# Kernel tuning notes

Measured on AMD Instinct MI355X. Metric: run time of the kernel, lower is better.

Reference implementation:

```python
import jax, jax.numpy as jnp
import numpy as np

B, S, D, H = 4, 1024, 1024, 16
HD = D // H  # head_dim = 64


def setup_inputs() -> dict:
    key = jax.random.key(0)
    ks = jax.random.split(key, 12)
    inp = {
        "query": jax.random.normal(ks[0], (B, S, D), jnp.float32),
        "key": jax.random.normal(ks[1], (B, S, D), jnp.float32),
        "value": jax.random.normal(ks[2], (B, S, D), jnp.float32),
        # padding mask: 0 = masked, 1 = keep; broadcastable to [B,H,Sq,Sk]
        "mask": jax.random.randint(ks[3], (B, 1, 1, S), 0, 2, jnp.int32),
        # Dense params (Glorot-ish scale)
        "Wq": jax.random.normal(ks[4], (D, D), jnp.float32) / np.sqrt(D),
        "bq": jnp.zeros((D,), jnp.float32),
        "Wk": jax.random.normal(ks[5], (D, D), jnp.float32) / np.sqrt(D),
        "bk": jnp.zeros((D,), jnp.float32),
        "Wv": jax.random.normal(ks[6], (D, D), jnp.float32) / np.sqrt(D),
        "bv": jnp.zeros((D,), jnp.float32),
        "Wo": jax.random.normal(ks[7], (D, D), jnp.float32) / np.sqrt(D),
        "bo": jnp.zeros((D,), jnp.float32),
    }
    return inp


def _split_heads(x):
    # [B, S, D] -> [B, H, S, HD]
    b, s, _ = x.shape
    return x.reshape(b, s, H, HD).transpose(0, 2, 1, 3)


def reference(query, key, value, mask, Wq, bq, Wk, bk, Wv, bv, Wo, bo):
    q = _split_heads(query @ Wq + bq)   # [B,H,S,HD]
    k = _split_heads(key @ Wk + bk)
    v = _split_heads(value @ Wv + bv)

    scale = jnp.sqrt(jnp.asarray(HD, q.dtype))
    energy = jnp.einsum("bhqd,bhkd->bhqk", q, k) / scale  # [B,H,S,S]
    energy = jnp.where(mask == 0, jnp.asarray(-1e10, energy.dtype), energy)
    attention = jax.nn.softmax(energy, axis=-1)
    # dropout is identity at inference
    x = jnp.einsum("bhqk,bhkd->bhqd", attention, v)       # [B,H,S,HD]
    x = x.transpose(0, 2, 1, 3).reshape(query.shape[0], -1, H * HD)  # [B,S,D]
    outputs = x @ Wo + bo
    return outputs, attention
```

## Files before the change

### kernel.cpp

```cpp
#include <hip/hip_runtime.h>

typedef short short8  __attribute__((ext_vector_type(8)));
typedef short short4v __attribute__((ext_vector_type(4)));
typedef float float4v __attribute__((ext_vector_type(4)));
typedef int   int4v   __attribute__((ext_vector_type(4)));

__device__ __forceinline__ short f2bf(float f) {
    unsigned u = __builtin_bit_cast(unsigned, f);
    u += 0x7fff + ((u >> 16) & 1);
    return (short)(u >> 16);
}

__device__ __forceinline__ void gl_lds16(const void* g, void* l) {
    __builtin_amdgcn_global_load_lds(
        (const __attribute__((address_space(1))) void*)g,
        (__attribute__((address_space(3))) void*)l, 16, 0, 0);
}

__global__ __launch_bounds__(256) void prep(
    const float* __restrict__ W0, const float* __restrict__ W1,
    const float* __restrict__ W2, const float* __restrict__ W3,
    short* __restrict__ T0, short* __restrict__ T1,
    short* __restrict__ T2, short* __restrict__ T3,
    const float* __restrict__ qf, const float* __restrict__ kf,
    const float* __restrict__ vf,
    short* __restrict__ Qb, short* __restrict__ Kb, short* __restrict__ Vb)
{
    __shared__ short Tl[64 * 72];
    const int tid = threadIdx.x;
    if (blockIdx.x >= 1024) {
        int cid = blockIdx.x - 1024;
        int arr = cid >> 11;
        const float* src = arr == 0 ? qf : arr == 1 ? kf : vf;
        short*       dst = arr == 0 ? Qb : arr == 1 ? Kb : Vb;
        size_t base = ((size_t)(cid & 2047) * 256 + tid) * 8;
        float4v v0 = *(const float4v*)&src[base];
        float4v v1 = *(const float4v*)&src[base + 4];
        short8 o = {f2bf(v0[0]), f2bf(v0[1]), f2bf(v0[2]), f2bf(v0[3]),
                    f2bf(v1[0]), f2bf(v1[1]), f2bf(v1[2]), f2bf(v1[3])};
        *(short8*)&dst[base] = o;
        return;
    }
    const int mat = blockIdx.x >> 8;
    const int t   = blockIdx.x & 255;
    const int k0 = (t >> 4) * 64, n0 = (t & 15) * 64;
    const float* W = mat == 0 ? W0 : mat == 1 ? W1 : mat == 2 ? W2 : W3;
    short*       T = mat == 0 ? T0 : mat == 1 ? T1 : mat == 2 ? T2 : T3;
    #pragma unroll
    for (int i = 0; i < 4; i++) {
        int c = tid + i * 256;
        int row = c >> 4, c4 = (c & 15) * 4;
        float4v v = *(const float4v*)&W[(size_t)(k0 + row) * 1024 + n0 + c4];
        short4v s = {f2bf(v[0]), f2bf(v[1]), f2bf(v[2]), f2bf(v[3])};
        *(short4v*)&Tl[row * 72 + c4] = s;
    }
    __syncthreads();
    #pragma unroll
    for (int i = 0; i < 2; i++) {
        int c = tid + i * 256;
        int nrow = c >> 3, k8 = (c & 7) * 8;
        short8 v;
        #pragma unroll
        for (int e = 0; e < 8; e++) v[e] = Tl[(k8 + e) * 72 + nrow];
        *(short8*)&T[(size_t)(n0 + nrow) * 1024 + k0 + k8] = v;
    }
}

template<int CMODE>
__global__ __launch_bounds__(256) void gemm128(
    const short* __restrict__ A, const short* __restrict__ Bt,
    const float* __restrict__ bias, void* __restrict__ Cv,
    int M, int N, int K)
{
    __shared__ short As[128 * 64];
    __shared__ short Bs[64 * 64];
    const int tid = threadIdx.x;
    const int w = tid >> 6, lid = tid & 63, quad = lid >> 4, l15 = lid & 15;
    const int wr = w >> 1, wc = w & 1;
    const int m0 = blockIdx.x * 128, n0 = blockIdx.y * 64;
    const int lrow = lid >> 3;
    const int lcb  = lid & 7;

    float4v acc[4][2];
    #pragma unroll
    for (int i = 0; i < 4; i++)
        #pragma unroll
        for (int j = 0; j < 2; j++) acc[i][j] = (float4v){0.f, 0.f, 0.f, 0.f};

    for (int kb = 0; kb < K; kb += 64) {
        #pragma unroll
        for (int p = 0; p < 4; p++) {
            int chunk = p * 4 + w;
            int row = chunk * 8 + lrow;
            int cb = lcb ^ (row & 7);
            gl_lds16(&A[(size_t)(m0 + row) * K + kb + cb * 8], &As[chunk * 512]);
        }
        #pragma unroll
        for (int p = 0; p < 2; p++) {
            int chunk = p * 4 + w;
            int row = chunk * 8 + lrow;
            int cb = lcb ^ (row & 7);
            gl_lds16(&Bt[(size_t)(n0 + row) * K + kb + cb * 8], &Bs[chunk * 512]);
        }
        __syncthreads();

        short8 af[4][2], bfr[2][2];
        #pragma unroll
        for (int i = 0; i < 4; i++) {
            int row = wr * 64 + i * 16 + l15;
            int sw = row & 7;
            #pragma unroll
            for (int h = 0; h < 2; h++)
                af[i][h] = *(short8*)&As[row * 64 + ((h * 4 + quad) ^ sw) * 8];
        }
        #pragma unroll
        for (int j = 0; j < 2; j++) {
            int row = wc * 32 + j * 16 + l15;
            int sw = row & 7;
            #pragma unroll
            for (int h = 0; h < 2; h++)
                bfr[j][h] = *(short8*)&Bs[row * 64 + ((h * 4 + quad) ^ sw) * 8];
        }
        #pragma unroll
        for (int i = 0; i < 4; i++)
            #pragma unroll
            for (int j = 0; j < 2; j++) {
                acc[i][j] = __builtin_amdgcn_mfma_f32_16x16x32_bf16(
                    af[i][0], bfr[j][0], acc[i][j], 0, 0, 0);
                acc[i][j] = __builtin_amdgcn_mfma_f32_16x16x32_bf16(
                    af[i][1], bfr[j][1], acc[i][j], 0, 0, 0);
            }
        __syncthreads();
    }

    #pragma unroll
    for (int j = 0; j < 2; j++) {
        int n = n0 + wc * 32 + j * 16 + l15;
        float bj = bias[n];
        #pragma unroll
        for (int i = 0; i < 4; i++) {
            if constexpr (CMODE == 2) {
                short* Vt = (short*)Cv;
                int b = m0 >> 10;
                int sbase = (m0 & 1023) + wr * 64 + i * 16 + quad * 4;
                short4v sv;
                #pragma unroll
                for (int r = 0; r < 4; r++) sv[r] = f2bf(acc[i][j][r] + bj);
                *(short4v*)&Vt[(size_t)b * 1048576 + (size_t)n * 1024 + sbase] = sv;
            } else {
                #pragma unroll
                for (int r = 0; r < 4; r++) {
                    int m = m0 + wr * 64 + i * 16 + quad * 4 + r;
                    if constexpr (CMODE == 1)
                        ((float*)Cv)[(size_t)m * N + n] = acc[i][j][r] + bj;
                    else
                        ((short*)Cv)[(size_t)m * N + n] = f2bf(acc[i][j][r] + bj);
                }
            }
        }
    }
}

__global__ __launch_bounds__(256) void attn_kernel(
    const short* __restrict__ Qp, const short* __restrict__ Kp,
    const short* __restrict__ Vt, const int* __restrict__ mask,
    float* __restrict__ attnOut, short* __restrict__ X)
{
    __shared__ short Pl[4][16][32];
    __shared__ int   maskl[1024];
    __shared__ float redmx[4][16];
    __shared__ float redsm[4][16];
    __shared__ float Xr[4][16][64];

    const int tid = threadIdx.x;
    const int w = tid >> 6, lid = tid & 63, quad = lid >> 4, l15 = lid & 15;
    const int bid = blockIdx.x;
    const int qb = bid & 63;
    const int bh = bid >> 6;
    const int b = bh >> 4, h = bh & 15;
    const int q0 = qb * 16;
    const size_t rowbase = (size_t)b * 1048576;
    const size_t hoff = (size_t)h * 64;

    *(int4v*)&maskl[tid * 4] = *(const int4v*)&mask[b * 1024 + tid * 4];

    short8 aq0 = *(const short8*)
        &Qp[rowbase + (size_t)(q0 + l15) * 1024 + hoff + quad * 8];
    short8 aq1 = *(const short8*)
        &Qp[rowbase + (size_t)(q0 + l15) * 1024 + hoff + 32 + quad * 8];

    float4v accS[16];
    #pragma unroll
    for (int a = 0; a < 16; a++) accS[a] = (float4v){0.f, 0.f, 0.f, 0.f};

    #pragma unroll
    for (int nk = 0; nk < 8; nk++) {
        #pragma unroll
        for (int jj = 0; jj < 2; jj++) {
            int n = nk * 128 + w * 32 + jj * 16 + l15;
            const short* kr = &Kp[rowbase + (size_t)n * 1024 + hoff + quad * 8];
            short8 b0 = *(const short8*)kr;
            short8 b1 = *(const short8*)(kr + 32);
            int a = nk * 2 + jj;
            accS[a] = __builtin_amdgcn_mfma_f32_16x16x32_bf16(aq0, b0, accS[a], 0, 0, 0);
            accS[a] = __builtin_amdgcn_mfma_f32_16x16x32_bf16(aq1, b1, accS[a], 0, 0, 0);
        }
    }
    __syncthreads();

    float mx[4] = {-3e38f, -3e38f, -3e38f, -3e38f};
    #pragma unroll
    for (int a = 0; a < 16; a++) {
        int col = (a >> 1) * 128 + w * 32 + (a & 1) * 16 + l15;
        bool keep = maskl[col] != 0;
        #pragma unroll
        for (int r = 0; r < 4; r++) {
            float s = accS[a][r] * 0.125f;
            s = keep ? s : -1e10f;
            accS[a][r] = s;
            mx[r] = fmaxf(mx[r], s);
        }
    }
    #pragma unroll
    for (int off = 1; off < 16; off <<= 1)
        #pragma unroll
        for (int r = 0; r < 4; r++) mx[r] = fmaxf(mx[r], __shfl_xor(mx[r], off));
    if (l15 == 0) {
        #pragma unroll
        for (int r = 0; r < 4; r++) redmx[w][quad * 4 + r] = mx[r];
    }
    __syncthreads();
    float mrow[4], sm[4] = {0.f, 0.f, 0.f, 0.f};
    #pragma unroll
    for (int r = 0; r < 4; r++) {
        int qr = quad * 4 + r;
        mrow[r] = fmaxf(fmaxf(redmx[0][qr], redmx[1][qr]),
                        fmaxf(redmx[2][qr], redmx[3][qr]));
    }
    #pragma unroll
    for (int a = 0; a < 16; a++)
        #pragma unroll
        for (int r = 0; r < 4; r++) {
            float e = __expf(accS[a][r] - mrow[r]);
            accS[a][r] = e;
            sm[r] += e;
        }
    #pragma unroll
    for (int off = 1; off < 16; off <<= 1)
        #pragma unroll
        for (int r = 0; r < 4; r++) sm[r] += __shfl_xor(sm[r], off);
    if (l15 == 0) {
        #pragma unroll
        for (int r = 0; r < 4; r++) redsm[w][quad * 4 + r] = sm[r];
    }
    __syncthreads();
    float inv[4];
    #pragma unroll
    for (int r = 0; r < 4; r++) {
        int qr = quad * 4 + r;
        inv[r] = 1.0f / (redsm[0][qr] + redsm[1][qr] + redsm[2][qr] + redsm[3][qr]);
    }

    const size_t abase = ((size_t)bh * 1024 + q0) * 1024;
    float4v accXp[4];
    #pragma unroll
    for (int jj = 0; jj < 4; jj++) accXp[jj] = (float4v){0.f, 0.f, 0.f, 0.f};

    for (int kt = 0; kt < 8; kt++) {
        #pragma unroll
        for (int jj2 = 0; jj2 < 2; jj2++) {
            int a = kt * 2 + jj2;
            int col = kt * 128 + w * 32 + jj2 * 16 + l15;
            #pragma unroll
            for (int r = 0; r < 4; r++) {
                float p = accS[a][r] * inv[r];
                attnOut[abase + (size_t)(quad * 4 + r) * 1024 + col] = p;
                Pl[w][quad * 4 + r][jj2 * 16 + l15] = f2bf(p);
            }
        }
        short8 ap = *(short8*)&Pl[w][l15][quad * 8];
        #pragma unroll
        for (int jj = 0; jj < 4; jj++) {
            short8 bv = *(const short8*)
                &Vt[rowbase + (hoff + jj * 16 + l15) * 1024 +
                    kt * 128 + w * 32 + quad * 8];
            accXp[jj] = __builtin_amdgcn_mfma_f32_16x16x32_bf16(ap, bv, accXp[jj], 0, 0, 0);
        }
    }

    #pragma unroll
    for (int jj = 0; jj < 4; jj++)
        #pragma unroll
        for (int r = 0; r < 4; r++)
            Xr[w][quad * 4 + r][jj * 16 + l15] = accXp[jj][r];
    __syncthreads();
    {
        int q = tid >> 4, d4 = (tid & 15) * 4;
        float4v s0 = *(float4v*)&Xr[0][q][d4];
        float4v s1 = *(float4v*)&Xr[1][q][d4];
        float4v s2 = *(float4v*)&Xr[2][q][d4];
        float4v s3 = *(float4v*)&Xr[3][q][d4];
        short4v o;
        #pragma unroll
        for (int e = 0; e < 4; e++)
            o[e] = f2bf(s0[e] + s1[e] + s2[e] + s3[e]);
        *(short4v*)&X[rowbase + (size_t)(q0 + q) * 1024 + hoff + d4] = o;
    }
}

extern "C" void kernel_launch(void* const* d_in, const int* in_sizes, int n_in,
                              void* d_out, int out_size, void* d_ws, size_t ws_size,
                              hipStream_t stream)
{
    const float* q_in = (const float*)d_in[0];
    const float* k_in = (const float*)d_in[1];
    const float* v_in = (const float*)d_in[2];
    const int*   mask = (const int*)d_in[3];
    const float* Wq = (const float*)d_in[4];
    const float* bq = (const float*)d_in[5];
    const float* Wk = (const float*)d_in[6];
    const float* bk = (const float*)d_in[7];
    const float* Wv = (const float*)d_in[8];
    const float* bv = (const float*)d_in[9];
    const float* Wo = (const float*)d_in[10];
    const float* bo = (const float*)d_in[11];

    short* ws = (short*)d_ws;
    const size_t MEL = 4096ull * 1024;
    short* Qp  = ws;
    short* Kp  = ws + MEL;
    short* Vt  = ws + 2 * MEL;
    short* Xp  = ws + 3 * MEL;
    short* WqT = ws + 4 * MEL;
    short* WkT = WqT + 1024 * 1024;
    short* WvT = WkT + 1024 * 1024;
    short* WoT = WvT + 1024 * 1024;

    float* outp  = (float*)d_out;
    float* attnp = outp + MEL;

    short* Qb = (short*)attnp;
    short* Kb = Qb + MEL;
    short* Vb = Kb + MEL;

    prep<<<dim3(7168), dim3(256), 0, stream>>>(Wq, Wk, Wv, Wo,
                                               WqT, WkT, WvT, WoT,
                                               q_in, k_in, v_in, Qb, Kb, Vb);
    dim3 gg(32, 16);
    gemm128<0><<<gg, 256, 0, stream>>>(Qb, WqT, bq, Qp, 4096, 1024, 1024);
    gemm128<0><<<gg, 256, 0, stream>>>(Kb, WkT, bk, Kp, 4096, 1024, 1024);
    gemm128<2><<<gg, 256, 0, stream>>>(Vb, WvT, bv, Vt, 4096, 1024, 1024);
    attn_kernel<<<dim3(4096), dim3(256), 0, stream>>>(Qp, Kp, Vt, mask, attnp, Xp);
    gemm128<1><<<gg, 256, 0, stream>>>(Xp, WoT, bo, outp, 4096, 1024, 1024);
}
```

Measured before the change: 529.6 us.

## Batch QKV GEMMs into one launch and coalesce attention-probability stores via LDS staging

The three projection GEMMs are merged into a single 3D-grid launch that picks operands by blockIdx.z, relying on Qb/Kb/Vb and WqT/WkT/WvT being laid out contiguously. This cuts launch overhead and gives one larger grid. In the attention kernel, normalized probabilities are staged in fp32 LDS with a padded stride and written to the attention output as coalesced float4 nontemporal stores, replacing scattered scalar stores. Two alternating LDS buffers and accumulator sets let consecutive tiles overlap, at the cost of extra LDS and registers.

Measured after the change: 499.9 us. 5.6% less time.

```diff
diff --git a/kernel.cpp b/kernel.cpp
--- a/kernel.cpp
+++ b/kernel.cpp
@@ -66,26 +66,14 @@
     }
 }
 
-template<int CMODE>
-__global__ __launch_bounds__(256) void gemm128(
+__device__ __forceinline__ void gemm_body(
     const short* __restrict__ A, const short* __restrict__ Bt,
-    const float* __restrict__ bias, void* __restrict__ Cv,
-    int M, int N, int K)
-{
-    __shared__ short As[128 * 64];
-    __shared__ short Bs[64 * 64];
+    short* As, short* Bs, float4v (&acc)[4][2], int m0, int n0, int K)
+{
     const int tid = threadIdx.x;
     const int w = tid >> 6, lid = tid & 63, quad = lid >> 4, l15 = lid & 15;
     const int wr = w >> 1, wc = w & 1;
-    const int m0 = blockIdx.x * 128, n0 = blockIdx.y * 64;
-    const int lrow = lid >> 3;
-    const int lcb  = lid & 7;
-
-    float4v acc[4][2];
-    #pragma unroll
-    for (int i = 0; i < 4; i++)
-        #pragma unroll
-        for (int j = 0; j < 2; j++) acc[i][j] = (float4v){0.f, 0.f, 0.f, 0.f};
+    const int lrow = lid >> 3, lcb = lid & 7;
 
     for (int kb = 0; kb < K; kb += 64) {
         #pragma unroll
@@ -132,32 +120,87 @@
             }
         __syncthreads();
     }
-
+}
+
+__global__ __launch_bounds__(256) void gemm_qkv(
+    const short* __restrict__ Ab, const short* __restrict__ Btb,
+    const float* __restrict__ b0, const float* __restrict__ b1,
+    const float* __restrict__ b2, short* __restrict__ Cq,
+    short* __restrict__ Ck, short* __restrict__ Cvt)
+{
+    __shared__ short As[128 * 64];
+    __shared__ short Bs[64 * 64];
+    const int zz = blockIdx.z;
+    const short* A  = Ab  + (size_t)zz * 4194304;
+    const short* Bt = Btb + (size_t)zz * 1048576;
+    const float* bias = zz == 0 ? b0 : zz == 1 ? b1 : b2;
+    const int m0 = blockIdx.x * 128, n0 = blockIdx.y * 64;
+
+    float4v acc[4][2];
+    #pragma unroll
+    for (int i = 0; i < 4; i++)
+        #pragma unroll
+        for (int j = 0; j < 2; j++) acc[i][j] = (float4v){0.f, 0.f, 0.f, 0.f};
+
+    gemm_body(A, Bt, As, Bs, acc, m0, n0, 1024);
+
+    const int tid = threadIdx.x;
+    const int w = tid >> 6, lid = tid & 63, quad = lid >> 4, l15 = lid & 15;
+    const int wr = w >> 1, wc = w & 1;
     #pragma unroll
     for (int j = 0; j < 2; j++) {
         int n = n0 + wc * 32 + j * 16 + l15;
         float bj = bias[n];
         #pragma unroll
         for (int i = 0; i < 4; i++) {
-            if constexpr (CMODE == 2) {
-                short* Vt = (short*)Cv;
+            if (zz == 2) {
                 int b = m0 >> 10;
                 int sbase = (m0 & 1023) + wr * 64 + i * 16 + quad * 4;
                 short4v sv;
                 #pragma unroll
                 for (int r = 0; r < 4; r++) sv[r] = f2bf(acc[i][j][r] + bj);
-                *(short4v*)&Vt[(size_t)b * 1048576 + (size_t)n * 1024 + sbase] = sv;
+                *(short4v*)&Cvt[(size_t)b * 1048576 + (size_t)n * 1024 + sbase] = sv;
             } else {
+                short* C = zz == 0 ? Cq : Ck;
                 #pragma unroll
                 for (int r = 0; r < 4; r++) {
                     int m = m0 + wr * 64 + i * 16 + quad * 4 + r;
-                    if constexpr (CMODE == 1)
-                        ((float*)Cv)[(size_t)m * N + n] = acc[i][j][r] + bj;
-                    else
-                        ((short*)Cv)[(size_t)m * N + n] = f2bf(acc[i][j][r] + bj);
+                    C[(size_t)m * 1024 + n] = f2bf(acc[i][j][r] + bj);
                 }
             }
         }
+    }
+}
+
+__global__ __launch_bounds__(256) void gemm_out(
+    const short* __restrict__ A, const short* __restrict__ Bt,
+    const float* __restrict__ bias, float* __restrict__ C)
+{
+    __shared__ short As[128 * 64];
+    __shared__ short Bs[64 * 64];
+    const int m0 = blockIdx.x * 128, n0 = blockIdx.y * 64;
+    float4v acc[4][2];
+    #pragma unroll
+    for (int i = 0; i < 4; i++)
+        #pragma unroll
+        for (int j = 0; j < 2; j++) acc[i][j] = (float4v){0.f, 0.f, 0.f, 0.f};
+
+    gemm_body(A, Bt, As, Bs, acc, m0, n0, 1024);
+
+    const int tid = threadIdx.x;
+    const int w = tid >> 6, lid = tid & 63, quad = lid >> 4, l15 = lid & 15;
+    const int wr = w >> 1, wc = w & 1;
+    #pragma unroll
+    for (int j = 0; j < 2; j++) {
+        int n = n0 + wc * 32 + j * 16 + l15;
+        float bj = bias[n];
+        #pragma unroll
+        for (int i = 0; i < 4; i++)
+            #pragma unroll
+            for (int r = 0; r < 4; r++) {
+                int m = m0 + wr * 64 + i * 16 + quad * 4 + r;
+                C[(size_t)m * 1024 + n] = acc[i][j][r] + bj;
+            }
     }
 }
 
@@ -166,11 +209,10 @@
     const short* __restrict__ Vt, const int* __restrict__ mask,
     float* __restrict__ attnOut, short* __restrict__ X)
 {
-    __shared__ short Pl[4][16][32];
+    __shared__ float SH[4608];
     __shared__ int   maskl[1024];
     __shared__ float redmx[4][16];
     __shared__ float redsm[4][16];
-    __shared__ float Xr[4][16][64];
 
     const int tid = threadIdx.x;
     const int w = tid >> 6, lid = tid & 63, quad = lid >> 4, l15 = lid & 15;
@@ -262,44 +304,65 @@
     }
 
     const size_t abase = ((size_t)bh * 1024 + q0) * 1024;
-    float4v accXp[4];
-    #pragma unroll
-    for (int jj = 0; jj < 4; jj++) accXp[jj] = (float4v){0.f, 0.f, 0.f, 0.f};
-
-    for (int kt = 0; kt < 8; kt++) {
-        #pragma unroll
-        for (int jj2 = 0; jj2 < 2; jj2++) {
-            int a = kt * 2 + jj2;
-            int col = kt * 128 + w * 32 + jj2 * 16 + l15;
-            #pragma unroll
-            for (int r = 0; r < 4; r++) {
-                float p = accS[a][r] * inv[r];
-                attnOut[abase + (size_t)(quad * 4 + r) * 1024 + col] = p;
-                Pl[w][quad * 4 + r][jj2 * 16 + l15] = f2bf(p);
-            }
-        }
-        short8 ap = *(short8*)&Pl[w][l15][quad * 8];
-        #pragma unroll
-        for (int jj = 0; jj < 4; jj++) {
-            short8 bv = *(const short8*)
-                &Vt[rowbase + (hoff + jj * 16 + l15) * 1024 +
-                    kt * 128 + w * 32 + quad * 8];
-            accXp[jj] = __builtin_amdgcn_mfma_f32_16x16x32_bf16(ap, bv, accXp[jj], 0, 0, 0);
-        }
-    }
-
+    float* Pw0 = &SH[(size_t)(0 * 4 + w) * 16 * 36];
+    float* Pw1 = &SH[(size_t)(1 * 4 + w) * 16 * 36];
+    float4v accA[4], accB[4];
+    #pragma unroll
+    for (int jj = 0; jj < 4; jj++) {
+        accA[jj] = (float4v){0.f, 0.f, 0.f, 0.f};
+        accB[jj] = (float4v){0.f, 0.f, 0.f, 0.f};
+    }
+
+    #pragma unroll
+    for (int t = 0; t < 4; t++) {
+        #pragma unroll
+        for (int par = 0; par < 2; par++) {
+            int kt = t * 2 + par;
+            float* Pw = par ? Pw1 : Pw0;
+            float4v* accp = par ? accB : accA;
+            #pragma unroll
+            for (int jj2 = 0; jj2 < 2; jj2++) {
+                int a = kt * 2 + jj2;
+                #pragma unroll
+                for (int r = 0; r < 4; r++)
+                    Pw[(quad * 4 + r) * 36 + jj2 * 16 + l15] = accS[a][r] * inv[r];
+            }
+            #pragma unroll
+            for (int pass = 0; pass < 2; pass++) {
+                int row = pass * 8 + (lid >> 3), c4 = (lid & 7) * 4;
+                float4v pv = *(float4v*)&Pw[row * 36 + c4];
+                __builtin_nontemporal_store(pv, (float4v*)
+                    &attnOut[abase + (size_t)row * 1024 + kt * 128 + w * 32 + c4]);
+            }
+            float4v pa0 = *(float4v*)&Pw[l15 * 36 + quad * 8];
+            float4v pa1 = *(float4v*)&Pw[l15 * 36 + quad * 8 + 4];
+            short8 ap = {f2bf(pa0[0]), f2bf(pa0[1]), f2bf(pa0[2]), f2bf(pa0[3]),
+                         f2bf(pa1[0]), f2bf(pa1[1]), f2bf(pa1[2]), f2bf(pa1[3])};
+            #pragma unroll
+            for (int jj = 0; jj < 4; jj++) {
+                short8 bv = *(const short8*)
+                    &Vt[rowbase + (hoff + jj * 16 + l15) * 1024 +
+                        kt * 128 + w * 32 + quad * 8];
+                accp[jj] = __builtin_amdgcn_mfma_f32_16x16x32_bf16(ap, bv, accp[jj], 0, 0, 0);
+            }
+        }
+    }
+
+    __syncthreads();
+    float* Xr = SH;
     #pragma unroll
     for (int jj = 0; jj < 4; jj++)
         #pragma unroll
         for (int r = 0; r < 4; r++)
-            Xr[w][quad * 4 + r][jj * 16 + l15] = accXp[jj][r];
+            Xr[(size_t)(w * 16 + quad * 4 + r) * 64 + jj * 16 + l15] =
+                accA[jj][r] + accB[jj][r];
     __syncthreads();
     {
         int q = tid >> 4, d4 = (tid & 15) * 4;
-        float4v s0 = *(float4v*)&Xr[0][q][d4];
-        float4v s1 = *(float4v*)&Xr[1][q][d4];
-        float4v s2 = *(float4v*)&Xr[2][q][d4];
-        float4v s3 = *(float4v*)&Xr[3][q][d4];
+        float4v s0 = *(float4v*)&Xr[(size_t)(0 * 16 + q) * 64 + d4];
+        float4v s1 = *(float4v*)&Xr[(size_t)(1 * 16 + q) * 64 + d4];
+        float4v s2 = *(float4v*)&Xr[(size_t)(2 * 16 + q) * 64 + d4];
+        float4v s3 = *(float4v*)&Xr[(size_t)(3 * 16 + q) * 64 + d4];
         short4v o;
         #pragma unroll
         for (int e = 0; e < 4; e++)
@@ -346,10 +409,8 @@
     prep<<<dim3(7168), dim3(256), 0, stream>>>(Wq, Wk, Wv, Wo,
                                                WqT, WkT, WvT, WoT,
                                                q_in, k_in, v_in, Qb, Kb, Vb);
-    dim3 gg(32, 16);
-    gemm128<0><<<gg, 256, 0, stream>>>(Qb, WqT, bq, Qp, 4096, 1024, 1024);
-    gemm128<0><<<gg, 256, 0, stream>>>(Kb, WkT, bk, Kp, 4096, 1024, 1024);
-    gemm128<2><<<gg, 256, 0, stream>>>(Vb, WvT, bv, Vt, 4096, 1024, 1024);
+    gemm_qkv<<<dim3(32, 16, 3), 256, 0, stream>>>(Qb, WqT, bq, bk, bv,
+                                                  Qp, Kp, Vt);
     attn_kernel<<<dim3(4096), dim3(256), 0, stream>>>(Qp, Kp, Vt, mask, attnp, Xp);
-    gemm128<1><<<gg, 256, 0, stream>>>(Xp, WoT, bo, outp, 4096, 1024, 1024);
-}
+    gemm_out<<<dim3(32, 16), 256, 0, stream>>>(Xp, WoT, bo, outp);
+}
```
